# Kernel optimization log

Measured on AMD Instinct MI355X. Metric: run time of the kernel, lower is better.

## Reference

```python
import jax, jax.numpy as jnp
import numpy as np
import math

B, S, D_MODEL, N_HEAD = 4, 2048, 1024, 16
D_K = D_MODEL // N_HEAD
ROPE_THETA = 10000.0


def _rope(x):
    # x: [B, H, S, Dk]; interleaved-pair rotary embedding.
    b, h, s, d = x.shape
    inv_freq = ROPE_THETA ** (-jnp.arange(0, d, 2, dtype=jnp.float32) / d)  # [d/2]
    ang = jnp.arange(s, dtype=jnp.float32)[:, None] * inv_freq[None, :]      # [S, d/2]
    cos, sin = jnp.cos(ang), jnp.sin(ang)
    x1, x2 = x[..., 0::2], x[..., 1::2]
    r1 = x1 * cos - x2 * sin
    r2 = x1 * sin + x2 * cos
    return jnp.stack([r1, r2], axis=-1).reshape(b, h, s, d)


def setup_inputs() -> dict:
    key = jax.random.key(0)
    ks = jax.random.split(key, 7)
    sc = 1.0 / math.sqrt(D_MODEL)
    return {
        "q": jax.random.normal(ks[0], (B, S, D_MODEL), jnp.float32),
        "k": jax.random.normal(ks[1], (B, S, D_MODEL), jnp.float32),
        "v": jax.random.normal(ks[2], (B, S, D_MODEL), jnp.float32),
        "Wq": jax.random.normal(ks[3], (D_MODEL, D_MODEL), jnp.float32) * sc,
        "Wk": jax.random.normal(ks[4], (D_MODEL, D_MODEL), jnp.float32) * sc,
        "Wv": jax.random.normal(ks[5], (D_MODEL, D_MODEL), jnp.float32) * sc,
        "Wo": jax.random.normal(ks[6], (D_MODEL, D_MODEL), jnp.float32) * sc,
    }


def _split(x):
    b, s, d = x.shape
    return x.reshape(b, s, N_HEAD, d // N_HEAD).transpose(0, 2, 1, 3)  # [B,H,S,Dk]


def reference(q, k, v, Wq, Wk, Wv, Wo):
    q = jnp.einsum("bsd,de->bse", q, Wq)
    k = jnp.einsum("bsd,de->bse", k, Wk)
    v = jnp.einsum("bsd,de->bse", v, Wv)
    qh, kh, vh = _split(q), _split(k), _split(v)
    qh, kh = _rope(qh), _rope(kh)
    scale = 1.0 / math.sqrt(D_K)
    score = jnp.einsum("bhqd,bhkd->bhqk", qh, kh) * scale  # [B,H,S,S]
    attn = jax.nn.softmax(score, axis=-1)
    out = jnp.einsum("bhqk,bhkd->bhqd", attn, vh)
    out = out.transpose(0, 2, 1, 3).reshape(q.shape[0], q.shape[1], D_MODEL)
    return jnp.einsum("bsd,de->bse", out, Wo)
```

## Files before the change

### kernel.cpp

```cpp
#include <hip/hip_runtime.h>
#include <stdint.h>

#define Bv 4
#define Sv 2048
#define Dv 1024
#define Hv 16
#define DKv 64
#define BSv (Bv * Sv)

typedef unsigned short u16;
typedef __attribute__((ext_vector_type(8))) short short8;
typedef __attribute__((ext_vector_type(8))) unsigned short u16x8;
typedef __attribute__((ext_vector_type(4))) unsigned short u16x4;
typedef __attribute__((ext_vector_type(4))) float f32x4;

__device__ __forceinline__ u16 f2bf(float f) {
  union { float f; uint32_t u; } x; x.f = f;
  uint32_t r = x.u + 0x7FFFu + ((x.u >> 16) & 1u);
  return (u16)(r >> 16);
}

__device__ __forceinline__ void gl_lds16(const void* g, void* l) {
  __builtin_amdgcn_global_load_lds(
      (__attribute__((address_space(1))) void*)g,
      (__attribute__((address_space(3))) void*)l, 16, 0, 0);
}

__device__ __forceinline__ f32x4 mfma16(short8 a, short8 b, f32x4 c) {
  return __builtin_amdgcn_mfma_f32_16x16x32_bf16(a, b, c, 0, 0, 0);
}

__global__ __launch_bounds__(256) void conv_qkv(
    const float* __restrict__ q, const float* __restrict__ k,
    const float* __restrict__ v, u16* __restrict__ qb, u16* __restrict__ kb,
    u16* __restrict__ vb) {
  const float* src = (blockIdx.y == 0) ? q : (blockIdx.y == 1 ? k : v);
  u16* dst = (blockIdx.y == 0) ? qb : (blockIdx.y == 1 ? kb : vb);
  int i = (blockIdx.x * 256 + threadIdx.x) * 8;
  const float4* s4 = (const float4*)(src + i);
  float4 a = s4[0], b = s4[1];
  u16x8 o = { f2bf(a.x), f2bf(a.y), f2bf(a.z), f2bf(a.w),
              f2bf(b.x), f2bf(b.y), f2bf(b.z), f2bf(b.w) };
  *(u16x8*)(dst + i) = o;
}

__global__ __launch_bounds__(256) void conv_wt(
    const float* __restrict__ w0, const float* __restrict__ w1,
    const float* __restrict__ w2, const float* __restrict__ w3,
    u16* __restrict__ t0, u16* __restrict__ t1, u16* __restrict__ t2,
    u16* __restrict__ t3) {
  const float* W = (blockIdx.z == 0) ? w0 : (blockIdx.z == 1 ? w1 : (blockIdx.z == 2 ? w2 : w3));
  u16* T = (blockIdx.z == 0) ? t0 : (blockIdx.z == 1 ? t1 : (blockIdx.z == 2 ? t2 : t3));
  __shared__ u16 tile[64][72];
  int nb = blockIdx.x * 64, kb = blockIdx.y * 64;
  int t = threadIdx.x;
#pragma unroll
  for (int p = 0; p < 4; ++p) {
    int idx = p * 256 + t;
    int r = idx >> 4;
    int c4 = (idx & 15) * 4;
    float4 vv = *(const float4*)(W + (size_t)(kb + r) * Dv + nb + c4);
    tile[c4 + 0][r] = f2bf(vv.x);
    tile[c4 + 1][r] = f2bf(vv.y);
    tile[c4 + 2][r] = f2bf(vv.z);
    tile[c4 + 3][r] = f2bf(vv.w);
  }
  __syncthreads();
#pragma unroll
  for (int p = 0; p < 4; ++p) {
    int idx = p * 256 + t;
    int r = idx >> 4;
    int c4 = (idx & 15) * 4;
    u16x4 o = { tile[r][c4], tile[r][c4 + 1], tile[r][c4 + 2], tile[r][c4 + 3] };
    *(u16x4*)(T + (size_t)(nb + r) * Dv + kb + c4) = o;
  }
}

__global__ __launch_bounds__(256) void gemm_bt(
    const u16* __restrict__ A, const u16* __restrict__ Bt,
    void* __restrict__ Out, int mode) {
  __shared__ u16 As[128 * 64];
  __shared__ u16 Bs[128 * 64];
  int tid = threadIdx.x;
  int lane = tid & 63, wid = tid >> 6;
  int quad = lane >> 4, cc = lane & 15;
  int wm = (wid >> 1) * 64, wn = (wid & 1) * 64;
  int m0 = blockIdx.x * 128, n0 = blockIdx.y * 128;

  f32x4 acc[4][4];
#pragma unroll
  for (int mi = 0; mi < 4; ++mi)
#pragma unroll
    for (int ni = 0; ni < 4; ++ni) {
      f32x4 z = {0.f, 0.f, 0.f, 0.f};
      acc[mi][ni] = z;
    }

  for (int k0 = 0; k0 < Dv; k0 += 64) {
#pragma unroll
    for (int p = 0; p < 4; ++p) {
      int slot = p * 256 + tid;
      int row = slot >> 3, cl = slot & 7;
      int cg = cl ^ (row & 7);
      gl_lds16(A + (size_t)(m0 + row) * Dv + k0 + cg * 8, &As[slot * 8]);
    }
#pragma unroll
    for (int p = 0; p < 4; ++p) {
      int slot = p * 256 + tid;
      int row = slot >> 3, cl = slot & 7;
      int cg = cl ^ (row & 7);
      gl_lds16(Bt + (size_t)(n0 + row) * Dv + k0 + cg * 8, &Bs[slot * 8]);
    }
    __syncthreads();
#pragma unroll
    for (int kk = 0; kk < 2; ++kk) {
      short8 af[4], bf[4];
#pragma unroll
      for (int mi = 0; mi < 4; ++mi) {
        int row = wm + mi * 16 + cc;
        int cg = kk * 4 + quad;
        af[mi] = *(const short8*)&As[row * 64 + (cg ^ (row & 7)) * 8];
      }
#pragma unroll
      for (int ni = 0; ni < 4; ++ni) {
        int row = wn + ni * 16 + cc;
        int cg = kk * 4 + quad;
        bf[ni] = *(const short8*)&Bs[row * 64 + (cg ^ (row & 7)) * 8];
      }
#pragma unroll
      for (int mi = 0; mi < 4; ++mi)
#pragma unroll
        for (int ni = 0; ni < 4; ++ni)
          acc[mi][ni] = mfma16(af[mi], bf[ni], acc[mi][ni]);
    }
    __syncthreads();
  }

  if (mode <= 1) {
    u16* O = (u16*)Out;
    float postscale = (mode == 0) ? 0.18033688011112042f : 1.0f;
#pragma unroll
    for (int ni = 0; ni < 4; ++ni) {
      int n = n0 + wn + ni * 16 + cc;
      int h = n >> 6, d = n & 63;
      float inv = __expf(-(float)(d & 62) * (9.210340372f / 64.0f));
      float sign = (d & 1) ? 1.0f : -1.0f;
#pragma unroll
      for (int mi = 0; mi < 4; ++mi) {
        int mB = m0 + wm + mi * 16 + quad * 4;
#pragma unroll
        for (int r = 0; r < 4; ++r) {
          int m = mB + r;
          int b = m >> 11, s = m & (Sv - 1);
          float val = acc[mi][ni][r];
          float part = __shfl_xor(val, 1);
          float sn, cs;
          __sincosf((float)s * inv, &sn, &cs);
          float outv = (val * cs + sign * part * sn) * postscale;
          O[((size_t)(b * Hv + h) * Sv + s) * DKv + d] = f2bf(outv);
        }
      }
    }
  } else if (mode == 2) {
    u16* O = (u16*)Out;
#pragma unroll
    for (int ni = 0; ni < 4; ++ni) {
      int n = n0 + wn + ni * 16 + cc;
      int h = n >> 6, d = n & 63;
#pragma unroll
      for (int mi = 0; mi < 4; ++mi) {
        int mB = m0 + wm + mi * 16 + quad * 4;
        int b = mB >> 11, s = mB & (Sv - 1);
        u16x4 o4 = { f2bf(acc[mi][ni][0]), f2bf(acc[mi][ni][1]),
                     f2bf(acc[mi][ni][2]), f2bf(acc[mi][ni][3]) };
        *(u16x4*)&O[((size_t)(b * Hv + h) * DKv + d) * Sv + s] = o4;
      }
    }
  } else {
    float* O = (float*)Out;
#pragma unroll
    for (int ni = 0; ni < 4; ++ni) {
      int n = n0 + wn + ni * 16 + cc;
#pragma unroll
      for (int mi = 0; mi < 4; ++mi) {
        int mB = m0 + wm + mi * 16 + quad * 4;
#pragma unroll
        for (int r = 0; r < 4; ++r)
          O[(size_t)(mB + r) * Dv + n] = acc[mi][ni][r];
      }
    }
  }
}

__global__ __launch_bounds__(256) void attn(
    const u16* __restrict__ Qp, const u16* __restrict__ Kp,
    const u16* __restrict__ Vt, u16* __restrict__ ctx) {
  __shared__ u16 Ks[2][64 * 64];
  __shared__ u16 Vs[2][64 * 64];
  __shared__ u16 Ps[4][64 * 72];
  int tid = threadIdx.x;
  int lane = tid & 63, wid = tid >> 6;
  int quad = lane >> 4, cc = lane & 15;
  int bh = blockIdx.y;
  int q0 = blockIdx.x * 256 + wid * 64;
  const u16* Qh = Qp + (size_t)bh * Sv * DKv;
  const u16* Kh = Kp + (size_t)bh * Sv * DKv;
  const u16* Vh = Vt + (size_t)bh * Sv * DKv;

  const short8 ones = { (short)0x3F80, (short)0x3F80, (short)0x3F80, (short)0x3F80,
                        (short)0x3F80, (short)0x3F80, (short)0x3F80, (short)0x3F80 };

  short8 qf[4][2];
#pragma unroll
  for (int mi = 0; mi < 4; ++mi)
#pragma unroll
    for (int kk = 0; kk < 2; ++kk)
      qf[mi][kk] = *(const short8*)&Qh[(size_t)(q0 + mi * 16 + cc) * DKv + kk * 32 + quad * 8];

  f32x4 o[4][4];
  f32x4 ol[4];
#pragma unroll
  for (int mi = 0; mi < 4; ++mi) {
#pragma unroll
    for (int nd = 0; nd < 4; ++nd) {
      f32x4 z = {0.f, 0.f, 0.f, 0.f};
      o[mi][nd] = z;
    }
    f32x4 z = {0.f, 0.f, 0.f, 0.f};
    ol[mi] = z;
  }

#pragma unroll
  for (int p = 0; p < 2; ++p) {
    int slot = p * 256 + tid;
    int row = slot >> 3, cl = slot & 7;
    int cg = cl ^ (row & 7);
    gl_lds16(Kh + (size_t)row * DKv + cg * 8, &Ks[0][slot * 8]);
    gl_lds16(Vh + (size_t)row * Sv + cg * 8, &Vs[0][slot * 8]);
  }

  for (int kt = 0; kt < Sv / 64; ++kt) {
    int cur = kt & 1;
    __syncthreads();

    if (kt + 1 < Sv / 64) {
      int s1 = (kt + 1) * 64;
#pragma unroll
      for (int p = 0; p < 2; ++p) {
        int slot = p * 256 + tid;
        int row = slot >> 3, cl = slot & 7;
        int cg = cl ^ (row & 7);
        gl_lds16(Kh + (size_t)(s1 + row) * DKv + cg * 8, &Ks[1 - cur][slot * 8]);
        gl_lds16(Vh + (size_t)row * Sv + s1 + cg * 8, &Vs[1 - cur][slot * 8]);
      }
    }

    short8 kf[4][2];
#pragma unroll
    for (int kc = 0; kc < 4; ++kc)
#pragma unroll
      for (int kk = 0; kk < 2; ++kk) {
        int row = kc * 16 + cc;
        int cg = kk * 4 + quad;
        kf[kc][kk] = *(const short8*)&Ks[cur][row * 64 + (cg ^ (row & 7)) * 8];
      }

#pragma unroll
    for (int mi = 0; mi < 4; ++mi) {
      f32x4 sc[4];
#pragma unroll
      for (int kc = 0; kc < 4; ++kc) {
        f32x4 z = {0.f, 0.f, 0.f, 0.f};
        sc[kc] = z;
      }
#pragma unroll
      for (int kk = 0; kk < 2; ++kk)
#pragma unroll
        for (int kc = 0; kc < 4; ++kc)
          sc[kc] = mfma16(qf[mi][kk], kf[kc][kk], sc[kc]);
#pragma unroll
      for (int kc = 0; kc < 4; ++kc)
#pragma unroll
        for (int r = 0; r < 4; ++r) {
          float pv = __builtin_amdgcn_exp2f(sc[kc][r]);
          Ps[wid][(mi * 16 + quad * 4 + r) * 72 + kc * 16 + cc] =
              (u16)(__float_as_uint(pv) >> 16);
        }
    }

#pragma unroll
    for (int kk = 0; kk < 2; ++kk) {
      short8 vf[4], pf[4];
#pragma unroll
      for (int nd = 0; nd < 4; ++nd) {
        int row = nd * 16 + cc;
        int cg = kk * 4 + quad;
        vf[nd] = *(const short8*)&Vs[cur][row * 64 + (cg ^ (row & 7)) * 8];
      }
#pragma unroll
      for (int mi = 0; mi < 4; ++mi)
        pf[mi] = *(const short8*)&Ps[wid][(mi * 16 + cc) * 72 + (kk * 4 + quad) * 8];
#pragma unroll
      for (int mi = 0; mi < 4; ++mi)
        ol[mi] = mfma16(pf[mi], ones, ol[mi]);
#pragma unroll
      for (int mi = 0; mi < 4; ++mi)
#pragma unroll
        for (int nd = 0; nd < 4; ++nd)
          o[mi][nd] = mfma16(pf[mi], vf[nd], o[mi][nd]);
    }
  }

  int b = bh >> 4, h = bh & 15;
#pragma unroll
  for (int mi = 0; mi < 4; ++mi)
#pragma unroll
    for (int r = 0; r < 4; ++r) {
      int s = q0 + mi * 16 + quad * 4 + r;
      float linv = 1.0f / ol[mi][r];
#pragma unroll
      for (int nd = 0; nd < 4; ++nd) {
        int d = h * DKv + nd * 16 + cc;
        ctx[((size_t)b * Sv + s) * Dv + d] = f2bf(o[mi][nd][r] * linv);
      }
    }
}

extern "C" void kernel_launch(void* const* d_in, const int* in_sizes, int n_in,
                              void* d_out, int out_size, void* d_ws, size_t ws_size,
                              hipStream_t stream) {
  (void)in_sizes; (void)n_in; (void)out_size; (void)ws_size;
  const float* q  = (const float*)d_in[0];
  const float* k  = (const float*)d_in[1];
  const float* v  = (const float*)d_in[2];
  const float* Wq = (const float*)d_in[3];
  const float* Wk = (const float*)d_in[4];
  const float* Wv = (const float*)d_in[5];
  const float* Wo = (const float*)d_in[6];

  char* ws = (char*)d_ws;
  size_t off = 0;
  const size_t big = (size_t)BSv * Dv * sizeof(u16);
  const size_t wsz = (size_t)Dv * Dv * sizeof(u16);
  u16* qb  = (u16*)(ws + off); off += big;
  u16* kb  = (u16*)(ws + off); off += big;
  u16* vb  = (u16*)(ws + off); off += big;
  u16* Wqt = (u16*)(ws + off); off += wsz;
  u16* Wkt = (u16*)(ws + off); off += wsz;
  u16* Wvt = (u16*)(ws + off); off += wsz;
  u16* Wot = (u16*)(ws + off); off += wsz;
  u16* Qp  = (u16*)(ws + off); off += big;
  u16* Kp  = (u16*)(ws + off); off += big;
  u16* Vtr = (u16*)(ws + off); off += big;
  u16* ctx = (u16*)(ws + off); off += big;

  conv_qkv<<<dim3(BSv * Dv / (256 * 8), 3), 256, 0, stream>>>(q, k, v, qb, kb, vb);
  conv_wt<<<dim3(Dv / 64, Dv / 64, 4), 256, 0, stream>>>(Wq, Wk, Wv, Wo, Wqt, Wkt, Wvt, Wot);
  gemm_bt<<<dim3(BSv / 128, Dv / 128), 256, 0, stream>>>(qb, Wqt, Qp, 0);
  gemm_bt<<<dim3(BSv / 128, Dv / 128), 256, 0, stream>>>(kb, Wkt, Kp, 1);
  gemm_bt<<<dim3(BSv / 128, Dv / 128), 256, 0, stream>>>(vb, Wvt, Vtr, 2);
  attn<<<dim3(Sv / 256, Bv * Hv), 256, 0, stream>>>(Qp, Kp, Vtr, ctx);
  gemm_bt<<<dim3(BSv / 128, Dv / 128), 256, 0, stream>>>(ctx, Wot, d_out, 3);
}
```

Measured before the change: 392.6 us.

## Switch attention kernel to 32x32x16 MFMA with transposed score tiles

Rewrites the attention inner loop to use 32x32x16 bf16 MFMA instead of 16x16x32. Scores are computed as K·Q^T, so each lane holds consecutive key columns and can pack exp values into 64-bit LDS stores with perm. The P buffer is shrunk and reused per 32-row query slice. The LDS swizzle is changed to avoid bank conflicts, and launch bounds request 2 blocks per CU. The intent is fewer MFMA issues, cheaper P staging and better occupancy, at the cost of larger per-lane accumulators and register pressure.

```diff
diff --git a/kernel.cpp b/kernel.cpp
--- a/kernel.cpp
+++ b/kernel.cpp
@@ -13,6 +13,7 @@
 typedef __attribute__((ext_vector_type(8))) unsigned short u16x8;
 typedef __attribute__((ext_vector_type(4))) unsigned short u16x4;
 typedef __attribute__((ext_vector_type(4))) float f32x4;
+typedef __attribute__((ext_vector_type(16))) float f32x16;
 
 __device__ __forceinline__ u16 f2bf(float f) {
   union { float f; uint32_t u; } x; x.f = f;
@@ -28,6 +29,9 @@
 
 __device__ __forceinline__ f32x4 mfma16(short8 a, short8 b, f32x4 c) {
   return __builtin_amdgcn_mfma_f32_16x16x32_bf16(a, b, c, 0, 0, 0);
+}
+__device__ __forceinline__ f32x16 mfma32(short8 a, short8 b, f32x16 c) {
+  return __builtin_amdgcn_mfma_f32_32x32x16_bf16(a, b, c, 0, 0, 0);
 }
 
 __global__ __launch_bounds__(256) void conv_qkv(
@@ -192,15 +196,16 @@
   }
 }
 
-__global__ __launch_bounds__(256) void attn(
+__global__ __launch_bounds__(256, 2) void attn(
     const u16* __restrict__ Qp, const u16* __restrict__ Kp,
     const u16* __restrict__ Vt, u16* __restrict__ ctx) {
   __shared__ u16 Ks[2][64 * 64];
   __shared__ u16 Vs[2][64 * 64];
-  __shared__ u16 Ps[4][64 * 72];
+  __shared__ u16 Ps[4][32 * 64];
   int tid = threadIdx.x;
   int lane = tid & 63, wid = tid >> 6;
-  int quad = lane >> 4, cc = lane & 15;
+  int hi = lane >> 5, c32 = lane & 31;
+  int sz = (c32 & 7) ^ ((c32 >> 3) & 3);
   int bh = blockIdx.y;
   int q0 = blockIdx.x * 256 + wid * 64;
   const u16* Qh = Qp + (size_t)bh * Sv * DKv;
@@ -210,31 +215,30 @@
   const short8 ones = { (short)0x3F80, (short)0x3F80, (short)0x3F80, (short)0x3F80,
                         (short)0x3F80, (short)0x3F80, (short)0x3F80, (short)0x3F80 };
 
-  short8 qf[4][2];
-#pragma unroll
-  for (int mi = 0; mi < 4; ++mi)
-#pragma unroll
-    for (int kk = 0; kk < 2; ++kk)
-      qf[mi][kk] = *(const short8*)&Qh[(size_t)(q0 + mi * 16 + cc) * DKv + kk * 32 + quad * 8];
-
-  f32x4 o[4][4];
-  f32x4 ol[4];
-#pragma unroll
-  for (int mi = 0; mi < 4; ++mi) {
-#pragma unroll
-    for (int nd = 0; nd < 4; ++nd) {
-      f32x4 z = {0.f, 0.f, 0.f, 0.f};
-      o[mi][nd] = z;
-    }
-    f32x4 z = {0.f, 0.f, 0.f, 0.f};
-    ol[mi] = z;
+  short8 qf[2][4];
+#pragma unroll
+  for (int qs = 0; qs < 2; ++qs)
+#pragma unroll
+    for (int kk = 0; kk < 4; ++kk)
+      qf[qs][kk] = *(const short8*)&Qh[(size_t)(q0 + qs * 32 + c32) * DKv + kk * 16 + hi * 8];
+
+  f32x16 o[2][2];
+  f32x16 ol[2];
+#pragma unroll
+  for (int qs = 0; qs < 2; ++qs) {
+#pragma unroll
+    for (int dt = 0; dt < 2; ++dt)
+#pragma unroll
+      for (int r = 0; r < 16; ++r) o[qs][dt][r] = 0.f;
+#pragma unroll
+    for (int r = 0; r < 16; ++r) ol[qs][r] = 0.f;
   }
 
 #pragma unroll
   for (int p = 0; p < 2; ++p) {
     int slot = p * 256 + tid;
     int row = slot >> 3, cl = slot & 7;
-    int cg = cl ^ (row & 7);
+    int cg = cl ^ ((row & 7) ^ ((row >> 3) & 3));
     gl_lds16(Kh + (size_t)row * DKv + cg * 8, &Ks[0][slot * 8]);
     gl_lds16(Vh + (size_t)row * Sv + cg * 8, &Vs[0][slot * 8]);
   }
@@ -249,79 +253,78 @@
       for (int p = 0; p < 2; ++p) {
         int slot = p * 256 + tid;
         int row = slot >> 3, cl = slot & 7;
-        int cg = cl ^ (row & 7);
+        int cg = cl ^ ((row & 7) ^ ((row >> 3) & 3));
         gl_lds16(Kh + (size_t)(s1 + row) * DKv + cg * 8, &Ks[1 - cur][slot * 8]);
         gl_lds16(Vh + (size_t)row * Sv + s1 + cg * 8, &Vs[1 - cur][slot * 8]);
       }
     }
 
-    short8 kf[4][2];
-#pragma unroll
-    for (int kc = 0; kc < 4; ++kc)
-#pragma unroll
-      for (int kk = 0; kk < 2; ++kk) {
-        int row = kc * 16 + cc;
-        int cg = kk * 4 + quad;
-        kf[kc][kk] = *(const short8*)&Ks[cur][row * 64 + (cg ^ (row & 7)) * 8];
-      }
-
-#pragma unroll
-    for (int mi = 0; mi < 4; ++mi) {
-      f32x4 sc[4];
-#pragma unroll
-      for (int kc = 0; kc < 4; ++kc) {
-        f32x4 z = {0.f, 0.f, 0.f, 0.f};
-        sc[kc] = z;
-      }
-#pragma unroll
-      for (int kk = 0; kk < 2; ++kk)
-#pragma unroll
-        for (int kc = 0; kc < 4; ++kc)
-          sc[kc] = mfma16(qf[mi][kk], kf[kc][kk], sc[kc]);
-#pragma unroll
-      for (int kc = 0; kc < 4; ++kc)
-#pragma unroll
-        for (int r = 0; r < 4; ++r) {
-          float pv = __builtin_amdgcn_exp2f(sc[kc][r]);
-          Ps[wid][(mi * 16 + quad * 4 + r) * 72 + kc * 16 + cc] =
-              (u16)(__float_as_uint(pv) >> 16);
+    short8 kf[2][4];
+#pragma unroll
+    for (int ks = 0; ks < 2; ++ks)
+#pragma unroll
+      for (int kk = 0; kk < 4; ++kk)
+        kf[ks][kk] = *(const short8*)&Ks[cur][(ks * 32 + c32) * 64 + (((kk * 2 + hi) ^ sz)) * 8];
+
+    short8 vf[2][4];
+
+#pragma unroll
+    for (int qs = 0; qs < 2; ++qs) {
+      f32x16 st[2];
+#pragma unroll
+      for (int ks = 0; ks < 2; ++ks)
+#pragma unroll
+        for (int r = 0; r < 16; ++r) st[ks][r] = 0.f;
+#pragma unroll
+      for (int kk = 0; kk < 4; ++kk)
+#pragma unroll
+        for (int ks = 0; ks < 2; ++ks)
+          st[ks] = mfma32(kf[ks][kk], qf[qs][kk], st[ks]);
+
+#pragma unroll
+      for (int ks = 0; ks < 2; ++ks)
+#pragma unroll
+        for (int g = 0; g < 4; ++g) {
+          float e0 = __builtin_amdgcn_exp2f(st[ks][4 * g + 0]);
+          float e1 = __builtin_amdgcn_exp2f(st[ks][4 * g + 1]);
+          float e2 = __builtin_amdgcn_exp2f(st[ks][4 * g + 2]);
+          float e3 = __builtin_amdgcn_exp2f(st[ks][4 * g + 3]);
+          uint32_t w0 = __builtin_amdgcn_perm(__float_as_uint(e1), __float_as_uint(e0), 0x07060302u);
+          uint32_t w1 = __builtin_amdgcn_perm(__float_as_uint(e3), __float_as_uint(e2), 0x07060302u);
+          uint2 w = { w0, w1 };
+          int ch = (ks * 4 + g) ^ sz;
+          *(uint2*)&Ps[wid][c32 * 64 + ch * 8 + hi * 4] = w;
         }
-    }
-
-#pragma unroll
-    for (int kk = 0; kk < 2; ++kk) {
-      short8 vf[4], pf[4];
-#pragma unroll
-      for (int nd = 0; nd < 4; ++nd) {
-        int row = nd * 16 + cc;
-        int cg = kk * 4 + quad;
-        vf[nd] = *(const short8*)&Vs[cur][row * 64 + (cg ^ (row & 7)) * 8];
-      }
-#pragma unroll
-      for (int mi = 0; mi < 4; ++mi)
-        pf[mi] = *(const short8*)&Ps[wid][(mi * 16 + cc) * 72 + (kk * 4 + quad) * 8];
-#pragma unroll
-      for (int mi = 0; mi < 4; ++mi)
-        ol[mi] = mfma16(pf[mi], ones, ol[mi]);
-#pragma unroll
-      for (int mi = 0; mi < 4; ++mi)
-#pragma unroll
-        for (int nd = 0; nd < 4; ++nd)
-          o[mi][nd] = mfma16(pf[mi], vf[nd], o[mi][nd]);
+
+      if (qs == 0) {
+#pragma unroll
+        for (int dt = 0; dt < 2; ++dt)
+#pragma unroll
+          for (int kk = 0; kk < 4; ++kk)
+            vf[dt][kk] = *(const short8*)&Vs[cur][(dt * 32 + c32) * 64 + (((kk * 2 + hi) ^ sz)) * 8];
+      }
+
+#pragma unroll
+      for (int kk = 0; kk < 4; ++kk) {
+        short8 pf = *(const short8*)&Ps[wid][c32 * 64 + (((kk * 2 + hi) ^ sz)) * 8];
+        ol[qs] = mfma32(pf, ones, ol[qs]);
+        o[qs][0] = mfma32(pf, vf[0][kk], o[qs][0]);
+        o[qs][1] = mfma32(pf, vf[1][kk], o[qs][1]);
+      }
     }
   }
 
   int b = bh >> 4, h = bh & 15;
 #pragma unroll
-  for (int mi = 0; mi < 4; ++mi)
-#pragma unroll
-    for (int r = 0; r < 4; ++r) {
-      int s = q0 + mi * 16 + quad * 4 + r;
-      float linv = 1.0f / ol[mi][r];
-#pragma unroll
-      for (int nd = 0; nd < 4; ++nd) {
-        int d = h * DKv + nd * 16 + cc;
-        ctx[((size_t)b * Sv + s) * Dv + d] = f2bf(o[mi][nd][r] * linv);
+  for (int qs = 0; qs < 2; ++qs)
+#pragma unroll
+    for (int r = 0; r < 16; ++r) {
+      int q = q0 + qs * 32 + (r & 3) + 8 * (r >> 2) + 4 * hi;
+      float linv = 1.0f / ol[qs][r];
+#pragma unroll
+      for (int dt = 0; dt < 2; ++dt) {
+        int d = h * DKv + dt * 32 + c32;
+        ctx[((size_t)b * Sv + q) * Dv + d] = f2bf(o[qs][dt][r] * linv);
       }
     }
 }
```

Measured after the change: 347.5 us. 11.5% less time.
